# Kernel optimization log

Measured on AMD Instinct MI355X. Metric: run time of the kernel, lower is better.

## Reference

```python
import jax, jax.numpy as jnp
import numpy as np

B, N, IN_F, OUT_F, H = 16, 1024, 256, 256, 4
D = OUT_F // H  # head_dim = 64
NEG_SLOPE = 0.2


def setup_inputs() -> dict:
    key = jax.random.key(0)
    k1, k2, k3 = jax.random.split(key, 3)
    h = jax.random.normal(k1, (B, N, IN_F), dtype=jnp.float32)
    mask = jnp.ones((B, N), dtype=jnp.int32)
    W = jax.random.normal(k2, (OUT_F, IN_F), dtype=jnp.float32) * (1.0 / np.sqrt(IN_F))
    a = jax.random.normal(k3, (2 * D, 1), dtype=jnp.float32) * 0.1
    return {"h": h, "mask": mask, "W": W, "a": a}


def reference(h, mask, W, a):
    # Wh = h @ W.T -> (B, N, OUT_F) -> (B, H, N, D)
    Wh = jnp.einsum('bnf,of->bno', h, W)
    Wh = Wh.reshape(h.shape[0], h.shape[1], H, D).transpose(0, 2, 1, 3)
    # Additive split: cat([Wh_i, Wh_j]) @ a == Wh_i @ a1 + Wh_j @ a2 (same math,
    # avoids the O(N^2 * 2D) concat tensor)
    a1 = a[:D, 0]  # (D,)
    a2 = a[D:, 0]  # (D,)
    s1 = jnp.einsum('bhnd,d->bhn', Wh, a1)  # score for node i
    s2 = jnp.einsum('bhnd,d->bhn', Wh, a2)  # score for node j
    e = s1[:, :, :, None] + s2[:, :, None, :]          # (B, H, N, N)
    e = jnp.where(e >= 0, e, NEG_SLOPE * e)            # LeakyReLU(0.2)
    node_mask = mask.astype(bool)                      # (B, N)
    mm = node_mask[:, None, :, None] & node_mask[:, None, None, :]  # (B,1,N,N)
    e = jnp.where(mm, e, -jnp.inf)
    attn = jax.nn.softmax(e, axis=-1)
    # dropout is identity in eval mode
    attn = jnp.where(mm, attn, 0.0)
    h_prime = jnp.einsum('bhij,bhjd->bhid', attn, Wh)  # (B, H, N, D)
    h_prime = h_prime.transpose(0, 2, 1, 3).reshape(h.shape[0], h.shape[1], OUT_F)
    return h_prime * mask.astype(h_prime.dtype)[:, :, None]
```

## Files before the change

### kernel.cpp

```cpp
#include <hip/hip_runtime.h>

typedef short short8 __attribute__((ext_vector_type(8)));
typedef float floatx4 __attribute__((ext_vector_type(4)));
typedef unsigned int u32;

#define NEG_SLOPE 0.2f

__device__ __forceinline__ u32 pk_rtne(float a, float b) {
    u32 ua = __float_as_uint(a); ua += 0x7fffu + ((ua >> 16) & 1u);
    u32 ub = __float_as_uint(b); ub += 0x7fffu + ((ub >> 16) & 1u);
    return __builtin_amdgcn_perm(ub, ua, 0x07060302);
}
__device__ __forceinline__ u32 pk_trunc(float a, float b) {
    return __builtin_amdgcn_perm(__float_as_uint(b), __float_as_uint(a), 0x07060302);
}
__device__ __forceinline__ void split_pk(float a, float b, u32& hi, u32& lo) {
    u32 ua = __float_as_uint(a), ub = __float_as_uint(b);
    hi = __builtin_amdgcn_perm(ub, ua, 0x07060302);
    float la = a - __uint_as_float(ua & 0xffff0000u);
    float lb = b - __uint_as_float(ub & 0xffff0000u);
    lo = __builtin_amdgcn_perm(__float_as_uint(lb), __float_as_uint(la), 0x07060302);
}
__device__ __forceinline__ void gl_lds16(const void* g, void* l) {
    __builtin_amdgcn_global_load_lds((__attribute__((address_space(1))) u32*)(void*)g,
                                     (__attribute__((address_space(3))) u32*)l, 16, 0, 0);
}

__global__ __launch_bounds__(256, 4) void k_wh(
    const float* __restrict__ hin, const int* __restrict__ mask,
    const float* __restrict__ W, const float* __restrict__ a,
    unsigned short* __restrict__ WhF, float2* __restrict__ E1F1,
    float2* __restrict__ E2F2)
{
    __shared__ unsigned short Ahi[64 * 72], Alo[64 * 72];
    __shared__ unsigned short Bhi[64 * 72], Blo[64 * 72];
    __shared__ float2 sred[2][64];

    const int t = threadIdx.x;
    const int bi = blockIdx.x;
    const int mtile = bi >> 2, cb = bi & 3;
    const int m0g = mtile * 64;
    const int b = m0g >> 10;
    const int i0 = m0g & 1023;
    const int b4h = b * 4 + cb;
    const int wid = t >> 6, lane = t & 63;
    const int wm = wid >> 1, wn = wid & 1;
    const int l15 = lane & 15, q = lane >> 4;

    floatx4 acc[2][2];
#pragma unroll
    for (int mt = 0; mt < 2; ++mt)
#pragma unroll
        for (int nt = 0; nt < 2; ++nt) {
            floatx4 z = {0.f, 0.f, 0.f, 0.f};
            acc[mt][nt] = z;
        }

    for (int kt = 0; kt < 4; ++kt) {
        const int k0 = kt * 64;
#pragma unroll
        for (int p = 0; p < 4; ++p) {
            int idx = t + 256 * p;
            int row = idx >> 4, c4 = idx & 15;
            float4 v = *(const float4*)&hin[((size_t)(m0g + row)) * 256 + k0 + c4 * 4];
            u32 h0, l0, h1, l1;
            split_pk(v.x, v.y, h0, l0);
            split_pk(v.z, v.w, h1, l1);
            *(uint2*)&Ahi[row * 72 + c4 * 4] = make_uint2(h0, h1);
            *(uint2*)&Alo[row * 72 + c4 * 4] = make_uint2(l0, l1);
        }
#pragma unroll
        for (int p = 0; p < 4; ++p) {
            int idx = t + 256 * p;
            int row = idx >> 4, c4 = idx & 15;
            float4 v = *(const float4*)&W[((size_t)(cb * 64 + row)) * 256 + k0 + c4 * 4];
            u32 h0, l0, h1, l1;
            split_pk(v.x, v.y, h0, l0);
            split_pk(v.z, v.w, h1, l1);
            *(uint2*)&Bhi[row * 72 + c4 * 4] = make_uint2(h0, h1);
            *(uint2*)&Blo[row * 72 + c4 * 4] = make_uint2(l0, l1);
        }
        __syncthreads();
#pragma unroll
        for (int ks = 0; ks < 2; ++ks) {
            short8 ah[2], al[2], bh[2], bl[2];
#pragma unroll
            for (int mt = 0; mt < 2; ++mt) {
                int r = wm * 32 + mt * 16 + l15;
                ah[mt] = *(const short8*)&Ahi[r * 72 + ks * 32 + q * 8];
                al[mt] = *(const short8*)&Alo[r * 72 + ks * 32 + q * 8];
            }
#pragma unroll
            for (int nt = 0; nt < 2; ++nt) {
                int r = wn * 32 + nt * 16 + l15;
                bh[nt] = *(const short8*)&Bhi[r * 72 + ks * 32 + q * 8];
                bl[nt] = *(const short8*)&Blo[r * 72 + ks * 32 + q * 8];
            }
#pragma unroll
            for (int mt = 0; mt < 2; ++mt)
#pragma unroll
                for (int nt = 0; nt < 2; ++nt) {
                    acc[mt][nt] = __builtin_amdgcn_mfma_f32_16x16x32_bf16(ah[mt], bh[nt], acc[mt][nt], 0, 0, 0);
                    acc[mt][nt] = __builtin_amdgcn_mfma_f32_16x16x32_bf16(ah[mt], bl[nt], acc[mt][nt], 0, 0, 0);
                    acc[mt][nt] = __builtin_amdgcn_mfma_f32_16x16x32_bf16(al[mt], bh[nt], acc[mt][nt], 0, 0, 0);
                }
        }
        __syncthreads();
    }

    const int c32 = (i0 + wm * 32) >> 5;
#pragma unroll
    for (int nt = 0; nt < 2; ++nt) {
        int nt_a = wn * 2 + nt;
        uint4 v;
        v.x = pk_rtne(acc[0][nt][0], acc[0][nt][1]);
        v.y = pk_rtne(acc[0][nt][2], acc[0][nt][3]);
        v.z = pk_rtne(acc[1][nt][0], acc[1][nt][1]);
        v.w = pk_rtne(acc[1][nt][2], acc[1][nt][3]);
        *(uint4*)&WhF[(size_t)(((b4h * 32 + c32) * 4 + nt_a) * 64 + lane) * 8] = v;
    }

    float a1v[2], a2v[2];
#pragma unroll
    for (int nt = 0; nt < 2; ++nt) {
        int d = wn * 32 + nt * 16 + l15;
        a1v[nt] = a[d];
        a2v[nt] = a[64 + d];
    }
    float s1p[2][4], s2p[2][4];
#pragma unroll
    for (int mt = 0; mt < 2; ++mt)
#pragma unroll
        for (int r = 0; r < 4; ++r) {
            s1p[mt][r] = acc[mt][0][r] * a1v[0] + acc[mt][1][r] * a1v[1];
            s2p[mt][r] = acc[mt][0][r] * a2v[0] + acc[mt][1][r] * a2v[1];
        }
#pragma unroll
    for (int off = 1; off <= 8; off <<= 1)
#pragma unroll
        for (int mt = 0; mt < 2; ++mt)
#pragma unroll
            for (int r = 0; r < 4; ++r) {
                s1p[mt][r] += __shfl_xor(s1p[mt][r], off, 64);
                s2p[mt][r] += __shfl_xor(s2p[mt][r], off, 64);
            }
    if (l15 == 0) {
#pragma unroll
        for (int mt = 0; mt < 2; ++mt)
#pragma unroll
            for (int r = 0; r < 4; ++r)
                sred[wn][wm * 32 + mt * 16 + q * 4 + r] = make_float2(s1p[mt][r], s2p[mt][r]);
    }
    __syncthreads();
    if (t < 64) {
        float s1 = sred[0][t].x + sred[1][t].x;
        float s2 = sred[0][t].y + sred[1][t].y;
        int i = i0 + t;
        E1F1[(size_t)b4h * 1024 + i] = make_float2(__expf(s1), __expf(NEG_SLOPE * s1));
        int mj = mask[b * 1024 + i];
        E2F2[(size_t)b4h * 1024 + i] =
            make_float2(mj ? __expf(s2) : 0.f, mj ? __expf(NEG_SLOPE * s2) : 0.f);
    }
}

__global__ __launch_bounds__(256, 4) void k_attn(
    const int* __restrict__ mask,
    const unsigned short* __restrict__ WhF,
    const float2* __restrict__ E1F1, const float2* __restrict__ E2F2,
    float* __restrict__ out)
{
    __shared__ unsigned short sB[2][8192];
    __shared__ float2 sEF[2][128];

    const int t = threadIdx.x;
    const int bi = blockIdx.x;
    const int ib = bi & 15, hh = (bi >> 4) & 3, b = bi >> 6;
    const int i0 = ib * 64;
    const int b4h = b * 4 + hh;
    const int wid = t >> 6, lane = t & 63;
    const int l15 = lane & 15, q = lane >> 4;
    const int iw = i0 + wid * 16;

    float2 e1 = E1F1[(size_t)b4h * 1024 + iw + l15];
    const float E1 = e1.x, F1 = e1.y;

    floatx4 acc[4];
#pragma unroll
    for (int nt = 0; nt < 4; ++nt) {
        floatx4 z = {0.f, 0.f, 0.f, 0.f};
        acc[nt] = z;
    }
    float rs = 0.f;

    const char* gbase = (const char*)WhF + (size_t)b4h * 131072;

    {
        const char* gp = gbase;
#pragma unroll
        for (int i = 0; i < 4; ++i)
            gl_lds16(gp + wid * 4096 + i * 1024 + lane * 16,
                     (char*)&sB[0][0] + wid * 4096 + i * 1024);
        if (t < 128) sEF[0][t] = E2F2[(size_t)b4h * 1024 + t];
    }

    for (int jt = 0; jt < 8; ++jt) {
        const int buf = jt & 1;
        __syncthreads();
        if (jt < 7) {
            const char* gp = gbase + (size_t)(jt + 1) * 16384;
#pragma unroll
            for (int i = 0; i < 4; ++i)
                gl_lds16(gp + wid * 4096 + i * 1024 + lane * 16,
                         (char*)&sB[buf ^ 1][0] + wid * 4096 + i * 1024);
            if (t < 128) sEF[buf ^ 1][t] = E2F2[(size_t)b4h * 1024 + (jt + 1) * 128 + t];
        }
#pragma unroll
        for (int ks = 0; ks < 4; ++ks) {
            const float4 eA0 = *(const float4*)&sEF[buf][ks * 32 + q * 4];
            const float4 eA1 = *(const float4*)&sEF[buf][ks * 32 + q * 4 + 2];
            const float4 eB0 = *(const float4*)&sEF[buf][ks * 32 + 16 + q * 4];
            const float4 eB1 = *(const float4*)&sEF[buf][ks * 32 + 16 + q * 4 + 2];
            float w0 = fmaxf(E1 * eA0.x, F1 * eA0.y);
            float w1 = fmaxf(E1 * eA0.z, F1 * eA0.w);
            float w2 = fmaxf(E1 * eA1.x, F1 * eA1.y);
            float w3 = fmaxf(E1 * eA1.z, F1 * eA1.w);
            float w4 = fmaxf(E1 * eB0.x, F1 * eB0.y);
            float w5 = fmaxf(E1 * eB0.z, F1 * eB0.w);
            float w6 = fmaxf(E1 * eB1.x, F1 * eB1.y);
            float w7 = fmaxf(E1 * eB1.z, F1 * eB1.w);
            union { short8 s; u32 u[4]; } af;
            af.u[0] = pk_trunc(w0, w1);
            af.u[1] = pk_trunc(w2, w3);
            af.u[2] = pk_trunc(w4, w5);
            af.u[3] = pk_trunc(w6, w7);
#pragma unroll
            for (int uu = 0; uu < 4; ++uu)
                rs += __uint_as_float(af.u[uu] << 16) +
                      __uint_as_float(af.u[uu] & 0xffff0000u);
#pragma unroll
            for (int nt = 0; nt < 4; ++nt) {
                short8 bf = *(const short8*)&sB[buf][(ks * 4 + nt) * 512 + lane * 8];
                acc[nt] = __builtin_amdgcn_mfma_f32_16x16x32_bf16(af.s, bf, acc[nt], 0, 0, 0);
            }
        }
    }

    rs += __shfl_xor(rs, 16, 64);
    rs += __shfl_xor(rs, 32, 64);

#pragma unroll
    for (int r = 0; r < 4; ++r) {
        int i = iw + q * 4 + r;
        float l = __shfl(rs, q * 4 + r, 64);
        int mi = mask[b * 1024 + i];
        float inv = (mi && l > 0.f) ? 1.0f / l : 0.f;
#pragma unroll
        for (int nt = 0; nt < 4; ++nt)
            out[((size_t)(b * 1024 + i)) * 256 + hh * 64 + nt * 16 + l15] = acc[nt][r] * inv;
    }
}

extern "C" void kernel_launch(void* const* d_in, const int* in_sizes, int n_in,
                              void* d_out, int out_size, void* d_ws, size_t ws_size,
                              hipStream_t stream) {
    const float* h = (const float*)d_in[0];
    const int* mask = (const int*)d_in[1];
    const float* W = (const float*)d_in[2];
    const float* a = (const float*)d_in[3];
    float* out = (float*)d_out;

    unsigned short* WhF = (unsigned short*)d_ws;
    float2* E1F1 = (float2*)((char*)d_ws + (size_t)64 * 32 * 4 * 64 * 8 * 2);
    float2* E2F2 = E1F1 + 64 * 1024;

    hipLaunchKernelGGL(k_wh, dim3(1024), dim3(256), 0, stream, h, mask, W, a, WhF, E1F1, E2F2);
    hipLaunchKernelGGL(k_attn, dim3(1024), dim3(256), 0, stream, mask, WhF, E1F1, E2F2, out);
}
```

Baseline: 109.2 us.

## Rewrite projection with single-bf16 MFMA and folded scores; use 32x32 MFMA attention

The projection kernel drops the three-MFMA hi/lo bf16 split and uses plain RTNE bf16 inputs. The attention scores are computed in fp32 by first folding a1/a2 into W (v = W^T a), so no cross-wave reduction is needed. W is staged once in swizzled LDS, while h rows feed the MFMA straight from global memory. The attention kernel moves to 32x32x16 MFMAs with 128-row tiles, computes the softmax denominator with an extra MFMA against a ones vector, and loads E2F2 through global_load_lds. The Wh layout changes to match. Precision of Wh drops to single bf16, and the grid halves with launch bounds of 2.

```diff
diff --git a/kernel.cpp b/kernel.cpp
--- a/kernel.cpp
+++ b/kernel.cpp
@@ -2,6 +2,7 @@
 
 typedef short short8 __attribute__((ext_vector_type(8)));
 typedef float floatx4 __attribute__((ext_vector_type(4)));
+typedef float floatx16 __attribute__((ext_vector_type(16)));
 typedef unsigned int u32;
 
 #define NEG_SLOPE 0.2f
@@ -13,13 +14,6 @@
 }
 __device__ __forceinline__ u32 pk_trunc(float a, float b) {
     return __builtin_amdgcn_perm(__float_as_uint(b), __float_as_uint(a), 0x07060302);
-}
-__device__ __forceinline__ void split_pk(float a, float b, u32& hi, u32& lo) {
-    u32 ua = __float_as_uint(a), ub = __float_as_uint(b);
-    hi = __builtin_amdgcn_perm(ub, ua, 0x07060302);
-    float la = a - __uint_as_float(ua & 0xffff0000u);
-    float lb = b - __uint_as_float(ub & 0xffff0000u);
-    lo = __builtin_amdgcn_perm(__float_as_uint(lb), __float_as_uint(la), 0x07060302);
 }
 __device__ __forceinline__ void gl_lds16(const void* g, void* l) {
     __builtin_amdgcn_global_load_lds((__attribute__((address_space(1))) u32*)(void*)g,
@@ -32,138 +26,117 @@
     unsigned short* __restrict__ WhF, float2* __restrict__ E1F1,
     float2* __restrict__ E2F2)
 {
-    __shared__ unsigned short Ahi[64 * 72], Alo[64 * 72];
-    __shared__ unsigned short Bhi[64 * 72], Blo[64 * 72];
-    __shared__ float2 sred[2][64];
+    __shared__ unsigned short sBF[8 * 4 * 64 * 8];
+    __shared__ float sV1[256], sV2[256];
 
     const int t = threadIdx.x;
     const int bi = blockIdx.x;
-    const int mtile = bi >> 2, cb = bi & 3;
+    const int mtile = bi & 255, hh = bi >> 8;
     const int m0g = mtile * 64;
-    const int b = m0g >> 10;
-    const int i0 = m0g & 1023;
-    const int b4h = b * 4 + cb;
+    const int b = m0g >> 10, i0 = m0g & 1023;
+    const int b4h = b * 4 + hh;
     const int wid = t >> 6, lane = t & 63;
-    const int wm = wid >> 1, wn = wid & 1;
     const int l15 = lane & 15, q = lane >> 4;
 
-    floatx4 acc[2][2];
-#pragma unroll
-    for (int mt = 0; mt < 2; ++mt)
-#pragma unroll
-        for (int nt = 0; nt < 2; ++nt) {
-            floatx4 z = {0.f, 0.f, 0.f, 0.f};
-            acc[mt][nt] = z;
-        }
-
-    for (int kt = 0; kt < 4; ++kt) {
-        const int k0 = kt * 64;
-#pragma unroll
-        for (int p = 0; p < 4; ++p) {
-            int idx = t + 256 * p;
-            int row = idx >> 4, c4 = idx & 15;
-            float4 v = *(const float4*)&hin[((size_t)(m0g + row)) * 256 + k0 + c4 * 4];
-            u32 h0, l0, h1, l1;
-            split_pk(v.x, v.y, h0, l0);
-            split_pk(v.z, v.w, h1, l1);
-            *(uint2*)&Ahi[row * 72 + c4 * 4] = make_uint2(h0, h1);
-            *(uint2*)&Alo[row * 72 + c4 * 4] = make_uint2(l0, l1);
-        }
-#pragma unroll
-        for (int p = 0; p < 4; ++p) {
-            int idx = t + 256 * p;
-            int row = idx >> 4, c4 = idx & 15;
-            float4 v = *(const float4*)&W[((size_t)(cb * 64 + row)) * 256 + k0 + c4 * 4];
-            u32 h0, l0, h1, l1;
-            split_pk(v.x, v.y, h0, l0);
-            split_pk(v.z, v.w, h1, l1);
-            *(uint2*)&Bhi[row * 72 + c4 * 4] = make_uint2(h0, h1);
-            *(uint2*)&Blo[row * 72 + c4 * 4] = make_uint2(l0, l1);
-        }
-        __syncthreads();
-#pragma unroll
-        for (int ks = 0; ks < 2; ++ks) {
-            short8 ah[2], al[2], bh[2], bl[2];
-#pragma unroll
-            for (int mt = 0; mt < 2; ++mt) {
-                int r = wm * 32 + mt * 16 + l15;
-                ah[mt] = *(const short8*)&Ahi[r * 72 + ks * 32 + q * 8];
-                al[mt] = *(const short8*)&Alo[r * 72 + ks * 32 + q * 8];
-            }
-#pragma unroll
-            for (int nt = 0; nt < 2; ++nt) {
-                int r = wn * 32 + nt * 16 + l15;
-                bh[nt] = *(const short8*)&Bhi[r * 72 + ks * 32 + q * 8];
-                bl[nt] = *(const short8*)&Blo[r * 72 + ks * 32 + q * 8];
-            }
-#pragma unroll
-            for (int mt = 0; mt < 2; ++mt)
-#pragma unroll
-                for (int nt = 0; nt < 2; ++nt) {
-                    acc[mt][nt] = __builtin_amdgcn_mfma_f32_16x16x32_bf16(ah[mt], bh[nt], acc[mt][nt], 0, 0, 0);
-                    acc[mt][nt] = __builtin_amdgcn_mfma_f32_16x16x32_bf16(ah[mt], bl[nt], acc[mt][nt], 0, 0, 0);
-                    acc[mt][nt] = __builtin_amdgcn_mfma_f32_16x16x32_bf16(al[mt], bh[nt], acc[mt][nt], 0, 0, 0);
-                }
-        }
-        __syncthreads();
-    }
-
-    const int c32 = (i0 + wm * 32) >> 5;
-#pragma unroll
-    for (int nt = 0; nt < 2; ++nt) {
-        int nt_a = wn * 2 + nt;
-        uint4 v;
-        v.x = pk_rtne(acc[0][nt][0], acc[0][nt][1]);
-        v.y = pk_rtne(acc[0][nt][2], acc[0][nt][3]);
-        v.z = pk_rtne(acc[1][nt][0], acc[1][nt][1]);
-        v.w = pk_rtne(acc[1][nt][2], acc[1][nt][3]);
-        *(uint4*)&WhF[(size_t)(((b4h * 32 + c32) * 4 + nt_a) * 64 + lane) * 8] = v;
-    }
-
-    float a1v[2], a2v[2];
-#pragma unroll
-    for (int nt = 0; nt < 2; ++nt) {
-        int d = wn * 32 + nt * 16 + l15;
-        a1v[nt] = a[d];
-        a2v[nt] = a[64 + d];
-    }
-    float s1p[2][4], s2p[2][4];
-#pragma unroll
-    for (int mt = 0; mt < 2; ++mt)
-#pragma unroll
-        for (int r = 0; r < 4; ++r) {
-            s1p[mt][r] = acc[mt][0][r] * a1v[0] + acc[mt][1][r] * a1v[1];
-            s2p[mt][r] = acc[mt][0][r] * a2v[0] + acc[mt][1][r] * a2v[1];
-        }
-#pragma unroll
-    for (int off = 1; off <= 8; off <<= 1)
-#pragma unroll
-        for (int mt = 0; mt < 2; ++mt)
-#pragma unroll
-            for (int r = 0; r < 4; ++r) {
-                s1p[mt][r] += __shfl_xor(s1p[mt][r], off, 64);
-                s2p[mt][r] += __shfl_xor(s2p[mt][r], off, 64);
-            }
-    if (l15 == 0) {
-#pragma unroll
-        for (int mt = 0; mt < 2; ++mt)
-#pragma unroll
-            for (int r = 0; r < 4; ++r)
-                sred[wn][wm * 32 + mt * 16 + q * 4 + r] = make_float2(s1p[mt][r], s2p[mt][r]);
-    }
+    sV1[t] = 0.f;
+    sV2[t] = 0.f;
     __syncthreads();
-    if (t < 64) {
-        float s1 = sred[0][t].x + sred[1][t].x;
-        float s2 = sred[0][t].y + sred[1][t].y;
-        int i = i0 + t;
-        E1F1[(size_t)b4h * 1024 + i] = make_float2(__expf(s1), __expf(NEG_SLOPE * s1));
+
+    float vp1[8] = {0, 0, 0, 0, 0, 0, 0, 0};
+    float vp2[8] = {0, 0, 0, 0, 0, 0, 0, 0};
+    {
+        const int c = t & 31;
+        const int rb = t >> 5;
+#pragma unroll
+        for (int i = 0; i < 8; ++i) {
+            int row = i * 8 + rb;
+            const float* gp = &W[((size_t)(hh * 64 + row)) * 256 + c * 8];
+            float4 w0 = *(const float4*)gp;
+            float4 w1 = *(const float4*)(gp + 4);
+            float a1r = a[row], a2r = a[64 + row];
+            vp1[0] += a1r * w0.x; vp1[1] += a1r * w0.y; vp1[2] += a1r * w0.z; vp1[3] += a1r * w0.w;
+            vp1[4] += a1r * w1.x; vp1[5] += a1r * w1.y; vp1[6] += a1r * w1.z; vp1[7] += a1r * w1.w;
+            vp2[0] += a2r * w0.x; vp2[1] += a2r * w0.y; vp2[2] += a2r * w0.z; vp2[3] += a2r * w0.w;
+            vp2[4] += a2r * w1.x; vp2[5] += a2r * w1.y; vp2[6] += a2r * w1.z; vp2[7] += a2r * w1.w;
+            uint4 pv;
+            pv.x = pk_rtne(w0.x, w0.y); pv.y = pk_rtne(w0.z, w0.w);
+            pv.z = pk_rtne(w1.x, w1.y); pv.w = pk_rtne(w1.z, w1.w);
+            int kt = c >> 2, qq = c & 3, nt = row >> 4, r15 = row & 15;
+            int idx16 = (kt * 4 + nt) * 64 + qq * 16 + r15;
+            *(uint4*)&sBF[(idx16 ^ kt) * 8] = pv;
+        }
+    }
+#pragma unroll
+    for (int j = 0; j < 8; ++j) {
+        vp1[j] += __shfl_xor(vp1[j], 32, 64);
+        vp2[j] += __shfl_xor(vp2[j], 32, 64);
+    }
+    if (lane < 32) {
+        const int c = t & 31;
+#pragma unroll
+        for (int j = 0; j < 8; ++j) {
+            atomicAdd(&sV1[c * 8 + j], vp1[j]);
+            atomicAdd(&sV2[c * 8 + j], vp2[j]);
+        }
+    }
+    __syncthreads();
+
+    floatx4 acc[4];
+#pragma unroll
+    for (int nt = 0; nt < 4; ++nt) {
+        floatx4 z = {0.f, 0.f, 0.f, 0.f};
+        acc[nt] = z;
+    }
+    float s1a = 0.f, s2a = 0.f;
+    const float* hrow = &hin[((size_t)(m0g + wid * 16 + l15)) * 256 + q * 8];
+#pragma unroll
+    for (int kt = 0; kt < 8; ++kt) {
+        float4 h0 = *(const float4*)(hrow + kt * 32);
+        float4 h1 = *(const float4*)(hrow + kt * 32 + 4);
+        float4 v1a = *(const float4*)&sV1[kt * 32 + q * 8];
+        float4 v1b = *(const float4*)&sV1[kt * 32 + q * 8 + 4];
+        float4 v2a = *(const float4*)&sV2[kt * 32 + q * 8];
+        float4 v2b = *(const float4*)&sV2[kt * 32 + q * 8 + 4];
+        s1a += h0.x * v1a.x + h0.y * v1a.y + h0.z * v1a.z + h0.w * v1a.w
+             + h1.x * v1b.x + h1.y * v1b.y + h1.z * v1b.z + h1.w * v1b.w;
+        s2a += h0.x * v2a.x + h0.y * v2a.y + h0.z * v2a.z + h0.w * v2a.w
+             + h1.x * v2b.x + h1.y * v2b.y + h1.z * v2b.z + h1.w * v2b.w;
+        union { short8 s; uint4 u; } af;
+        af.u.x = pk_rtne(h0.x, h0.y); af.u.y = pk_rtne(h0.z, h0.w);
+        af.u.z = pk_rtne(h1.x, h1.y); af.u.w = pk_rtne(h1.z, h1.w);
+#pragma unroll
+        for (int nt = 0; nt < 4; ++nt) {
+            int idx16 = (kt * 4 + nt) * 64 + lane;
+            short8 bf = *(const short8*)&sBF[(idx16 ^ kt) * 8];
+            acc[nt] = __builtin_amdgcn_mfma_f32_16x16x32_bf16(af.s, bf, acc[nt], 0, 0, 0);
+        }
+    }
+
+    const int jt16 = (i0 >> 4) + wid;
+    const int g = q & 1, jb = (q >> 1) * 4;
+#pragma unroll
+    for (int nt = 0; nt < 4; ++nt) {
+        int nt32 = nt >> 1;
+        int l31 = (nt & 1) * 16 + l15;
+        uint2 pv;
+        pv.x = pk_rtne(acc[nt][0], acc[nt][1]);
+        pv.y = pk_rtne(acc[nt][2], acc[nt][3]);
+        size_t idx = ((((size_t)b4h * 64 + jt16) * 2 + nt32) * 64 + (g * 32 + l31)) * 8 + jb;
+        *(uint2*)&WhF[idx] = pv;
+    }
+
+    s1a += __shfl_xor(s1a, 16, 64); s1a += __shfl_xor(s1a, 32, 64);
+    s2a += __shfl_xor(s2a, 16, 64); s2a += __shfl_xor(s2a, 32, 64);
+    if (lane < 16) {
+        int i = i0 + wid * 16 + lane;
+        E1F1[(size_t)b4h * 1024 + i] = make_float2(__expf(s1a), __expf(NEG_SLOPE * s1a));
         int mj = mask[b * 1024 + i];
         E2F2[(size_t)b4h * 1024 + i] =
-            make_float2(mj ? __expf(s2) : 0.f, mj ? __expf(NEG_SLOPE * s2) : 0.f);
-    }
-}
-
-__global__ __launch_bounds__(256, 4) void k_attn(
+            make_float2(mj ? __expf(s2a) : 0.f, mj ? __expf(NEG_SLOPE * s2a) : 0.f);
+    }
+}
+
+__global__ __launch_bounds__(256, 2) void k_attn(
     const int* __restrict__ mask,
     const unsigned short* __restrict__ WhF,
     const float2* __restrict__ E1F1, const float2* __restrict__ E2F2,
@@ -174,33 +147,31 @@
 
     const int t = threadIdx.x;
     const int bi = blockIdx.x;
-    const int ib = bi & 15, hh = (bi >> 4) & 3, b = bi >> 6;
-    const int i0 = ib * 64;
-    const int b4h = b * 4 + hh;
+    const int b4h = bi & 63, ib = bi >> 6;
+    const int b = b4h >> 2, hh = b4h & 3;
+    const int i0 = ib * 128;
     const int wid = t >> 6, lane = t & 63;
-    const int l15 = lane & 15, q = lane >> 4;
-    const int iw = i0 + wid * 16;
-
-    float2 e1 = E1F1[(size_t)b4h * 1024 + iw + l15];
+    const int l31 = lane & 31, g = lane >> 5;
+    const int iw = i0 + wid * 32;
+
+    float2 e1 = E1F1[(size_t)b4h * 1024 + iw + l31];
     const float E1 = e1.x, F1 = e1.y;
 
-    floatx4 acc[4];
-#pragma unroll
-    for (int nt = 0; nt < 4; ++nt) {
-        floatx4 z = {0.f, 0.f, 0.f, 0.f};
-        acc[nt] = z;
-    }
-    float rs = 0.f;
+    floatx16 acc0, acc1, accL;
+#pragma unroll
+    for (int r = 0; r < 16; ++r) { acc0[r] = 0.f; acc1[r] = 0.f; accL[r] = 0.f; }
+    const short ob = (short)0x3F80;
+    const short8 ones = {ob, ob, ob, ob, ob, ob, ob, ob};
 
     const char* gbase = (const char*)WhF + (size_t)b4h * 131072;
 
     {
-        const char* gp = gbase;
 #pragma unroll
         for (int i = 0; i < 4; ++i)
-            gl_lds16(gp + wid * 4096 + i * 1024 + lane * 16,
+            gl_lds16(gbase + wid * 4096 + i * 1024 + lane * 16,
                      (char*)&sB[0][0] + wid * 4096 + i * 1024);
-        if (t < 128) sEF[0][t] = E2F2[(size_t)b4h * 1024 + t];
+        if (wid == 1)
+            gl_lds16((const char*)&E2F2[(size_t)b4h * 1024] + lane * 16, (char*)&sEF[0][0]);
     }
 
     for (int jt = 0; jt < 8; ++jt) {
@@ -212,14 +183,16 @@
             for (int i = 0; i < 4; ++i)
                 gl_lds16(gp + wid * 4096 + i * 1024 + lane * 16,
                          (char*)&sB[buf ^ 1][0] + wid * 4096 + i * 1024);
-            if (t < 128) sEF[buf ^ 1][t] = E2F2[(size_t)b4h * 1024 + (jt + 1) * 128 + t];
-        }
-#pragma unroll
-        for (int ks = 0; ks < 4; ++ks) {
-            const float4 eA0 = *(const float4*)&sEF[buf][ks * 32 + q * 4];
-            const float4 eA1 = *(const float4*)&sEF[buf][ks * 32 + q * 4 + 2];
-            const float4 eB0 = *(const float4*)&sEF[buf][ks * 32 + 16 + q * 4];
-            const float4 eB1 = *(const float4*)&sEF[buf][ks * 32 + 16 + q * 4 + 2];
+            if (wid == 1)
+                gl_lds16((const char*)&E2F2[(size_t)b4h * 1024 + (jt + 1) * 128] + lane * 16,
+                         (char*)&sEF[buf ^ 1][0]);
+        }
+#pragma unroll
+        for (int tl = 0; tl < 8; ++tl) {
+            const float4 eA0 = *(const float4*)&sEF[buf][tl * 16 + g * 4];
+            const float4 eA1 = *(const float4*)&sEF[buf][tl * 16 + g * 4 + 2];
+            const float4 eB0 = *(const float4*)&sEF[buf][tl * 16 + 8 + g * 4];
+            const float4 eB1 = *(const float4*)&sEF[buf][tl * 16 + 8 + g * 4 + 2];
             float w0 = fmaxf(E1 * eA0.x, F1 * eA0.y);
             float w1 = fmaxf(E1 * eA0.z, F1 * eA0.w);
             float w2 = fmaxf(E1 * eA1.x, F1 * eA1.y);
@@ -233,30 +206,24 @@
             af.u[1] = pk_trunc(w2, w3);
             af.u[2] = pk_trunc(w4, w5);
             af.u[3] = pk_trunc(w6, w7);
-#pragma unroll
-            for (int uu = 0; uu < 4; ++uu)
-                rs += __uint_as_float(af.u[uu] << 16) +
-                      __uint_as_float(af.u[uu] & 0xffff0000u);
-#pragma unroll
-            for (int nt = 0; nt < 4; ++nt) {
-                short8 bf = *(const short8*)&sB[buf][(ks * 4 + nt) * 512 + lane * 8];
-                acc[nt] = __builtin_amdgcn_mfma_f32_16x16x32_bf16(af.s, bf, acc[nt], 0, 0, 0);
-            }
-        }
-    }
-
-    rs += __shfl_xor(rs, 16, 64);
-    rs += __shfl_xor(rs, 32, 64);
-
-#pragma unroll
-    for (int r = 0; r < 4; ++r) {
-        int i = iw + q * 4 + r;
-        float l = __shfl(rs, q * 4 + r, 64);
+            short8 bf0 = *(const short8*)&sB[buf][((tl * 2 + 0) * 64 + lane) * 8];
+            short8 bf1 = *(const short8*)&sB[buf][((tl * 2 + 1) * 64 + lane) * 8];
+            acc0 = __builtin_amdgcn_mfma_f32_32x32x16_bf16(af.s, bf0, acc0, 0, 0, 0);
+            acc1 = __builtin_amdgcn_mfma_f32_32x32x16_bf16(af.s, bf1, acc1, 0, 0, 0);
+            accL = __builtin_amdgcn_mfma_f32_32x32x16_bf16(af.s, ones, accL, 0, 0, 0);
+        }
+    }
+
+#pragma unroll
+    for (int r = 0; r < 16; ++r) {
+        int row = (r & 3) + 8 * (r >> 2) + 4 * g;
+        int i = iw + row;
+        float l = accL[r];
         int mi = mask[b * 1024 + i];
         float inv = (mi && l > 0.f) ? 1.0f / l : 0.f;
-#pragma unroll
-        for (int nt = 0; nt < 4; ++nt)
-            out[((size_t)(b * 1024 + i)) * 256 + hh * 64 + nt * 16 + l15] = acc[nt][r] * inv;
+        size_t o = ((size_t)(b * 1024 + i)) * 256 + hh * 64;
+        out[o + l31] = acc0[r] * inv;
+        out[o + 32 + l31] = acc1[r] * inv;
     }
 }
 
@@ -270,9 +237,9 @@
     float* out = (float*)d_out;
 
     unsigned short* WhF = (unsigned short*)d_ws;
-    float2* E1F1 = (float2*)((char*)d_ws + (size_t)64 * 32 * 4 * 64 * 8 * 2);
+    float2* E1F1 = (float2*)((char*)d_ws + (size_t)64 * 64 * 2 * 64 * 8 * 2);
     float2* E2F2 = E1F1 + 64 * 1024;
 
     hipLaunchKernelGGL(k_wh, dim3(1024), dim3(256), 0, stream, h, mask, W, a, WhF, E1F1, E2F2);
-    hipLaunchKernelGGL(k_attn, dim3(1024), dim3(256), 0, stream, mask, WhF, E1F1, E2F2, out);
-}
+    hipLaunchKernelGGL(k_attn, dim3(512), dim3(256), 0, stream, mask, WhF, E1F1, E2F2, out);
+}
```

After: 104.3 us. -4.5%, faster.
